# Kernel optimization log

Hardware: AMD Instinct MI355X
Metric: run time of the kernel (lower is better)

## Reference

```python
import jax, jax.numpy as jnp
import numpy as np

B, S, D = 2, 2048, 2048
H, KVH, DH = 16, 4, 128  # n_heads, n_kv_heads, head_dim
N_REP = H // KVH
THETA = 10000.0


def setup_inputs() -> dict:
    key = jax.random.key(0)
    ks = jax.random.split(key, 6)
    x = jax.random.normal(ks[0], (B, S, D), dtype=jnp.float32)
    wq = jax.random.normal(ks[1], (H * DH, D), dtype=jnp.float32) * (D ** -0.5)
    wk = jax.random.normal(ks[2], (KVH * DH, D), dtype=jnp.float32) * (D ** -0.5)
    wv = jax.random.normal(ks[3], (KVH * DH, D), dtype=jnp.float32) * (D ** -0.5)
    wo = jax.random.normal(ks[4], (D, H * DH), dtype=jnp.float32) * (D ** -0.5)
    # RoPE frequencies (complex freqs -> cos/sin), shape [S, DH//2]
    inv_freq = 1.0 / (THETA ** (np.arange(0, DH, 2, dtype=np.float32) / DH))
    angles = np.arange(S, dtype=np.float32)[:, None] * inv_freq[None, :]
    freqs_cos = jnp.asarray(np.cos(angles))
    freqs_sin = jnp.asarray(np.sin(angles))
    # causal additive mask [1,1,S,S]
    neg = jnp.full((S, S), -1e9, dtype=jnp.float32)
    mask = jnp.triu(neg, k=1)[None, None]
    return {"x": x, "freqs_cos": freqs_cos, "freqs_sin": freqs_sin,
            "mask": mask, "wq": wq, "wk": wk, "wv": wv, "wo": wo}


def _rope(t, cos, sin):
    # t: [B,S,h,DH]; cos/sin: [S,DH//2] -> broadcast [1,S,1,DH//2]
    tp = t.reshape(*t.shape[:-1], -1, 2)
    tr, ti = tp[..., 0], tp[..., 1]
    c = cos[None, :, None, :]
    s = sin[None, :, None, :]
    out_r = tr * c - ti * s
    out_i = tr * s + ti * c
    return jnp.stack([out_r, out_i], axis=-1).reshape(t.shape)


def reference(x, freqs_cos, freqs_sin, mask, wq, wk, wv, wo):
    b, s, _ = x.shape
    xq = jnp.einsum('bsd,ed->bse', x, wq).reshape(b, s, H, DH)
    xk = jnp.einsum('bsd,ed->bse', x, wk).reshape(b, s, KVH, DH)
    xv = jnp.einsum('bsd,ed->bse', x, wv).reshape(b, s, KVH, DH)
    xq = _rope(xq, freqs_cos, freqs_sin)
    xk = _rope(xk, freqs_cos, freqs_sin)
    # GQA: repeat kv heads
    xk = jnp.repeat(xk, N_REP, axis=2)
    xv = jnp.repeat(xv, N_REP, axis=2)
    q = xq.transpose(0, 2, 1, 3)  # [B,H,S,DH]
    k = xk.transpose(0, 2, 1, 3)
    v = xv.transpose(0, 2, 1, 3)
    scores = jnp.einsum('bhqd,bhkd->bhqk', q, k) / jnp.sqrt(jnp.float32(DH))
    scores = scores + mask
    attn = jax.nn.softmax(scores.astype(jnp.float32), axis=-1).astype(q.dtype)
    out = jnp.einsum('bhqk,bhkd->bhqd', attn, v)
    out = out.transpose(0, 2, 1, 3).reshape(b, s, H * DH)
    return jnp.einsum('bse,de->bsd', out, wo)
```

## Files before the change

kernel.cpp:

```cpp
#include <hip/hip_runtime.h>

#define Bq   2
#define Sq   2048
#define Dq   2048
#define Hq   16
#define KVHq 4
#define DHq  128

typedef unsigned short u16;
typedef short  bf16x8 __attribute__((ext_vector_type(8)));
typedef float  f32x4  __attribute__((ext_vector_type(4)));
typedef float  f32x16 __attribute__((ext_vector_type(16)));
typedef unsigned short u16x2 __attribute__((ext_vector_type(2)));
typedef unsigned short u16x4 __attribute__((ext_vector_type(4)));

__device__ __forceinline__ u16 f2bf(float f) {
    unsigned u = __float_as_uint(f);
    u += 0x7fffu + ((u >> 16) & 1u);
    return (u16)(u >> 16);
}
__device__ __forceinline__ float bf2f(u16 s) {
    return __uint_as_float(((unsigned)s) << 16);
}

__global__ void cast_bf16(const float* __restrict__ in, u16* __restrict__ out, int n4) {
    int i = blockIdx.x * 256 + threadIdx.x;
    if (i >= n4) return;
    float4 v = ((const float4*)in)[i];
    u16x4 o;
    o.x = f2bf(v.x); o.y = f2bf(v.y); o.z = f2bf(v.z); o.w = f2bf(v.w);
    ((u16x4*)out)[i] = o;
}

__global__ void cast_weights(const float* __restrict__ wq, const float* __restrict__ wk,
                             const float* __restrict__ wv, const float* __restrict__ wo,
                             u16* __restrict__ wqb, u16* __restrict__ wkvb,
                             u16* __restrict__ wob) {
    int i = blockIdx.x * 256 + threadIdx.x;
    const float4* src; u16x4* dst; int off;
    if (i < 1048576)      { src = (const float4*)wq; dst = (u16x4*)wqb;  off = i; }
    else if (i < 1310720) { src = (const float4*)wk; dst = (u16x4*)wkvb; off = i - 1048576; }
    else if (i < 1572864) { src = (const float4*)wv; dst = (u16x4*)wkvb + 262144; off = i - 1310720; }
    else                  { src = (const float4*)wo; dst = (u16x4*)wob;  off = i - 1572864; }
    float4 v = src[off];
    u16x4 o;
    o.x = f2bf(v.x); o.y = f2bf(v.y); o.z = f2bf(v.z); o.w = f2bf(v.w);
    dst[off] = o;
}

__device__ __forceinline__ void async16(const void* g, void* l) {
    __builtin_amdgcn_global_load_lds(
        (const __attribute__((address_space(1))) unsigned*)g,
        (__attribute__((address_space(3))) unsigned*)l, 16, 0, 0);
}

__device__ __forceinline__ void stc(u16* p, float v)   { *p = f2bf(v); }
__device__ __forceinline__ void stc(float* p, float v) { *p = v; }

template <typename OutT>
__global__ __launch_bounds__(256) void gemm_nt(
    const u16* __restrict__ A, const u16* __restrict__ W, OutT* __restrict__ C,
    int M, int N, int K)
{
    __shared__ __align__(16) u16 lA[128 * 32];
    __shared__ __align__(16) u16 lB[128 * 32];

    const int t    = threadIdx.x;
    const int w    = t >> 6;
    const int lane = t & 63;
    const int lr   = lane & 15;
    const int quad = lane >> 4;
    const int wm   = (w >> 1) * 64, wn = (w & 1) * 64;
    const int bm   = blockIdx.x * 128, bn = blockIdx.y * 128;

    const u16* Ab = A + (size_t)bm * K;
    const u16* Wb = W + (size_t)bn * K;

    const int r0  = t >> 2;
    const int r1  = (256 + t) >> 2;
    const int kc0 = (t & 3) * 8;

    char* la0 = (char*)lA + w * 1024;
    char* la1 = (char*)lA + 4096 + w * 1024;
    char* lb0 = (char*)lB + w * 1024;
    char* lb1 = (char*)lB + 4096 + w * 1024;

    f32x4 acc[4][4] = {};

    for (int kt = 0; kt < K; kt += 32) {
        async16(Ab + (size_t)r0 * K + kt + kc0, la0);
        async16(Ab + (size_t)r1 * K + kt + kc0, la1);
        async16(Wb + (size_t)r0 * K + kt + kc0, lb0);
        async16(Wb + (size_t)r1 * K + kt + kc0, lb1);
        __syncthreads();

        bf16x8 af[4], bfr[4];
#pragma unroll
        for (int i = 0; i < 4; i++)
            af[i] = *(const bf16x8*)&lA[(wm + i * 16 + lr) * 32 + quad * 8];
#pragma unroll
        for (int j = 0; j < 4; j++)
            bfr[j] = *(const bf16x8*)&lB[(wn + j * 16 + lr) * 32 + quad * 8];
#pragma unroll
        for (int i = 0; i < 4; i++)
#pragma unroll
            for (int j = 0; j < 4; j++)
                acc[i][j] = __builtin_amdgcn_mfma_f32_16x16x32_bf16(af[i], bfr[j], acc[i][j], 0, 0, 0);
        __syncthreads();
    }

#pragma unroll
    for (int i = 0; i < 4; i++)
#pragma unroll
        for (int j = 0; j < 4; j++)
#pragma unroll
            for (int r = 0; r < 4; r++) {
                int gm = bm + wm + i * 16 + quad * 4 + r;
                int gn = bn + wn + j * 16 + lr;
                stc(C + (size_t)gm * N + gn, acc[i][j][r]);
            }
}

__global__ void rope_k(u16* __restrict__ T, const float* __restrict__ Cs,
                       const float* __restrict__ Sn, int lognh, int total) {
    int i = blockIdx.x * 256 + threadIdx.x;
    if (i >= total) return;
    int p  = i & 63;
    int sh = i >> 6;
    int s  = (sh >> lognh) & (Sq - 1);
    float c = Cs[s * 64 + p], sn = Sn[s * 64 + p];
    u16x2* ptr = ((u16x2*)T) + i;
    u16x2 v = *ptr;
    float tr = bf2f(v.x), ti = bf2f(v.y);
    u16x2 ov;
    ov.x = f2bf(tr * c - ti * sn);
    ov.y = f2bf(tr * sn + ti * c);
    *ptr = ov;
}

__global__ void rope_kv(u16* __restrict__ KV, const float* __restrict__ Cs,
                        const float* __restrict__ Sn, int total) {
    int i = blockIdx.x * 256 + threadIdx.x;
    if (i >= total) return;
    int p     = i & 63;
    int kvh   = (i >> 6) & 3;
    int token = i >> 8;
    int s     = token & (Sq - 1);
    float c = Cs[s * 64 + p], sn = Sn[s * 64 + p];
    u16x2* ptr = ((u16x2*)KV) + (size_t)token * 512 + kvh * 64 + p;
    u16x2 v = *ptr;
    float tr = bf2f(v.x), ti = bf2f(v.y);
    u16x2 ov;
    ov.x = f2bf(tr * c - ti * sn);
    ov.y = f2bf(tr * sn + ti * c);
    *ptr = ov;
}

__global__ void transpose_v_k(const u16* __restrict__ KV, u16* __restrict__ Vt) {
    __shared__ u16 tile[32][33];
    const int bk = blockIdx.z;
    const int b = bk >> 2, kvh = bk & 3;
    const int s0 = blockIdx.x * 32, d0 = blockIdx.y * 32;
    const int tx = threadIdx.x, ty = threadIdx.y;
    tile[ty][tx] = KV[(size_t)(b * Sq + s0 + ty) * 1024 + 512 + kvh * 128 + d0 + tx];
    __syncthreads();
    Vt[((size_t)bk * DHq + d0 + ty) * Sq + s0 + tx] = tile[tx][ty];
}

#define PSCALE 0.12753102f
#define PBIAS  17.31234049f

__global__ __launch_bounds__(256, 2) void flash_attn_sk2(
    const u16* __restrict__ Q, const u16* __restrict__ KV,
    const u16* __restrict__ Vt, float* __restrict__ Oc, float* __restrict__ Lc)
{
    __shared__ __align__(16) u16 kl[4 * 64 * 32];
    __shared__ __align__(16) u16 vl[2 * 128 * 32];
    __shared__ __align__(16) u16 pl[4][32 * 64];

    const int bh = blockIdx.x;
    const int b = bh >> 4, h = bh & 15;
    const int kvh = h >> 2;
    const int c = 39 - (int)blockIdx.y;
    int qt, ci, nc;
    if (c < 4)       { qt = c;                    ci = 0;            nc = 1; }
    else if (c < 12) { qt = 4  + ((c - 4) >> 1);  ci = (c - 4) & 1;  nc = 2; }
    else if (c < 24) { qt = 8  + (c - 12) / 3;    ci = (c - 12) % 3; nc = 3; }
    else             { qt = 12 + ((c - 24) >> 2); ci = (c - 24) & 3; nc = 4; }
    const int T  = 2 * (qt + 1);
    const int t0 = (ci * T) / nc, t1 = ((ci + 1) * T) / nc;

    const int tid = threadIdx.x;
    const int w = tid >> 6, lane = tid & 63;
    const int col = lane & 31, hi = lane >> 5;
    const int q0 = qt * 128 + w * 32;

    const u16* Qp = Q + (size_t)(b * Sq + q0 + col) * (Hq * DHq) + h * DHq + hi * 8;
    bf16x8 qf[8];
#pragma unroll
    for (int ks = 0; ks < 8; ks++) qf[ks] = *(const bf16x8*)(Qp + ks * 16);

    const u16* Kg = KV + (size_t)b * Sq * 1024 + kvh * DHq;
    const u16* Vg = Vt + (size_t)(b * KVHq + kvh) * DHq * Sq;

    const int srow = lane >> 2;
    const int swl  = ((lane & 3) ^ ((lane >> 3) & 3)) * 8;
    const int xsw  = (col >> 1) & 3;
    const int px   = col & 7;

    f32x16 o[4] = {};
    float lsum[16] = {};

    for (int kt = t0; kt < t1; kt++) {
        const int kb = kt * 64;
#pragma unroll
        for (int c4 = 0; c4 < 4; c4++) {
            const u16* g = Kg + (size_t)(kb + w * 16 + srow) * 1024 + c4 * 32 + swl;
            async16(g, (char*)kl + (c4 * 2048 + w * 512) * 2 + lane * 16);
        }
#pragma unroll
        for (int c4 = 0; c4 < 4; c4++) {
            const int g2 = c4 & 1, dbase = (c4 >> 1) * 64;
            const u16* g = Vg + (size_t)(dbase + w * 16 + srow) * Sq + kb + g2 * 32 + swl;
            async16(g, (char*)vl + (g2 * 4096 + (dbase + w * 16) * 32) * 2 + lane * 16);
        }
        __syncthreads();

        f32x16 s0 = {}, s1 = {};
#pragma unroll
        for (int ks = 0; ks < 8; ks++) {
            const int ch    = (((ks & 1) * 2 + hi) ^ xsw) * 8;
            const int kkbase = (ks >> 1) * 2048 + ch;
            bf16x8 k0 = *(const bf16x8*)&kl[kkbase + col * 32];
            bf16x8 k1 = *(const bf16x8*)&kl[kkbase + (32 + col) * 32];
            s0 = __builtin_amdgcn_mfma_f32_32x32x16_bf16(qf[ks], k0, s0, 0, 0, 0);
            s1 = __builtin_amdgcn_mfma_f32_32x32x16_bf16(qf[ks], k1, s1, 0, 0, 0);
        }

#pragma unroll
        for (int r = 0; r < 16; r++) {
            const int rloc = (r & 3) + 8 * (r >> 2) + 4 * hi;
            const int qg = q0 + rloc;
            float v0 = s0[r] * PSCALE - PBIAS;
            float v1 = s1[r] * PSCALE - PBIAS;
            float p0 = (kb + col      <= qg) ? exp2f(v0) : 0.f;
            float p1 = (kb + 32 + col <= qg) ? exp2f(v1) : 0.f;
            lsum[r] += p0 + p1;
            const int rx = rloc & 7;
            pl[w][rloc * 64 + (((col >> 3) ^ rx) * 8) + (col & 7)]       = f2bf(p0);
            pl[w][rloc * 64 + ((((col >> 3) + 4) ^ rx) * 8) + (col & 7)] = f2bf(p1);
        }

#pragma unroll
        for (int ks = 0; ks < 4; ks++) {
            bf16x8 pa = *(const bf16x8*)&pl[w][col * 64 + ((ks * 2 + hi) ^ px) * 8];
            const int vch   = (((ks & 1) * 2 + hi) ^ xsw) * 8;
            const int vbase = (ks >> 1) * 4096 + vch;
#pragma unroll
            for (int n = 0; n < 4; n++) {
                bf16x8 vf = *(const bf16x8*)&vl[vbase + (n * 32 + col) * 32];
                o[n] = __builtin_amdgcn_mfma_f32_32x32x16_bf16(pa, vf, o[n], 0, 0, 0);
            }
        }
        __syncthreads();
    }

    float* Ocb = Oc + (size_t)(bh * 40 + c) * 16384 + (size_t)w * 32 * 128;
    float* Lcb = Lc + (size_t)(bh * 40 + c) * 128 + w * 32;
#pragma unroll
    for (int r = 0; r < 16; r++) {
        const int rloc = (r & 3) + 8 * (r >> 2) + 4 * hi;
        float t = lsum[r];
        t += __shfl_xor(t, 1);
        t += __shfl_xor(t, 2);
        t += __shfl_xor(t, 4);
        t += __shfl_xor(t, 8);
        t += __shfl_xor(t, 16);
        if (col == 0) Lcb[rloc] = t;
#pragma unroll
        for (int n = 0; n < 4; n++)
            Ocb[rloc * 128 + n * 32 + col] = o[n][r];
    }
}

__global__ __launch_bounds__(256) void flash_reduce2(
    const float* __restrict__ Oc, const float* __restrict__ Lc, u16* __restrict__ AO)
{
    const int bh = blockIdx.x;
    const int qt = blockIdx.y;
    const int e  = blockIdx.z * 256 + threadIdx.x;
    const int row = e >> 5, col4 = e & 31;
    int cst, nc;
    if (qt < 4)       { cst = qt;                 nc = 1; }
    else if (qt < 8)  { cst = 4  + 2 * (qt - 4);  nc = 2; }
    else if (qt < 12) { cst = 12 + 3 * (qt - 8);  nc = 3; }
    else              { cst = 24 + 4 * (qt - 12); nc = 4; }
    f32x4 acc = {0.f, 0.f, 0.f, 0.f};
    float l = 0.f;
    for (int i = 0; i < nc; i++) {
        const size_t base = (size_t)(bh * 40 + cst + i);
        acc += ((const f32x4*)(Oc + base * 16384))[e];
        l   += Lc[base * 128 + row];
    }
    const float inv = 1.0f / l;
    const int b = bh >> 4, h = bh & 15;
    u16x4 ov;
    ov.x = f2bf(acc[0] * inv); ov.y = f2bf(acc[1] * inv);
    ov.z = f2bf(acc[2] * inv); ov.w = f2bf(acc[3] * inv);
    u16* dst = AO + (size_t)(b * Sq + qt * 128 + row) * (Hq * DHq) + h * DHq + col4 * 4;
    *(u16x4*)dst = ov;
}

__global__ __launch_bounds__(256) void flash_attn(
    const u16* __restrict__ Q, const u16* __restrict__ KV,
    const u16* __restrict__ Vt, u16* __restrict__ O)
{
    __shared__ __align__(16) u16 plds[4][16 * 72];
    const int bh = blockIdx.x;
    const int b = bh >> 4, h = bh & 15;
    const int kvh = h >> 2;
    const int w = threadIdx.x >> 6, lane = threadIdx.x & 63;
    const int lr = lane & 15, quad = lane >> 4;
    const int yy = gridDim.y - 1 - blockIdx.y;
    const int q0 = yy * 64 + w * 16;

    const u16* Qp = Q + (size_t)(b * Sq + q0 + lr) * (Hq * DHq) + h * DHq + quad * 8;
    bf16x8 qf[4];
#pragma unroll
    for (int kk = 0; kk < 4; kk++) qf[kk] = *(const bf16x8*)(Qp + kk * 32);

    const u16* Kp = KV + (size_t)b * Sq * 1024 + kvh * DHq;
    const u16* Vp = Vt + (size_t)(b * KVHq + kvh) * DHq * Sq;

    f32x4 o[8] = {};
    float lsum[4] = {0.f, 0.f, 0.f, 0.f};

    const int nt = (q0 + 16 + 63) >> 6;
    for (int kt = 0; kt < nt; kt++) {
        const int kb = kt * 64;
        f32x4 s[4] = {};
#pragma unroll
        for (int kk = 0; kk < 4; kk++) {
#pragma unroll
            for (int j = 0; j < 4; j++) {
                bf16x8 kf = *(const bf16x8*)(Kp + (size_t)(kb + j * 16 + lr) * 1024 + kk * 32 + quad * 8);
                s[j] = __builtin_amdgcn_mfma_f32_16x16x32_bf16(qf[kk], kf, s[j], 0, 0, 0);
            }
        }
#pragma unroll
        for (int r = 0; r < 4; r++) {
            const int qg = q0 + quad * 4 + r;
#pragma unroll
            for (int j = 0; j < 4; j++) {
                float v = s[j][r] * PSCALE - PBIAS;
                float p = (kb + j * 16 + lr <= qg) ? exp2f(v) : 0.f;
                lsum[r] += p;
                plds[w][(quad * 4 + r) * 72 + j * 16 + lr] = f2bf(p);
            }
        }
        bf16x8 pa0 = *(const bf16x8*)&plds[w][lr * 72 + quad * 8];
        bf16x8 pa1 = *(const bf16x8*)&plds[w][lr * 72 + 32 + quad * 8];
#pragma unroll
        for (int dt = 0; dt < 8; dt++) {
            bf16x8 v0 = *(const bf16x8*)(Vp + (size_t)(dt * 16 + lr) * Sq + kb + quad * 8);
            bf16x8 v1 = *(const bf16x8*)(Vp + (size_t)(dt * 16 + lr) * Sq + kb + 32 + quad * 8);
            o[dt] = __builtin_amdgcn_mfma_f32_16x16x32_bf16(pa0, v0, o[dt], 0, 0, 0);
            o[dt] = __builtin_amdgcn_mfma_f32_16x16x32_bf16(pa1, v1, o[dt], 0, 0, 0);
        }
    }

    u16* Ob = O + (size_t)(b * Sq) * (Hq * DHq) + h * DHq;
#pragma unroll
    for (int r = 0; r < 4; r++) {
        float t = lsum[r];
        t += __shfl_xor(t, 1);
        t += __shfl_xor(t, 2);
        t += __shfl_xor(t, 4);
        t += __shfl_xor(t, 8);
        const float inv = 1.0f / t;
        const int qg = q0 + quad * 4 + r;
#pragma unroll
        for (int dt = 0; dt < 8; dt++)
            Ob[(size_t)qg * (Hq * DHq) + dt * 16 + lr] = f2bf(o[dt][r] * inv);
    }
}

extern "C" void kernel_launch(void* const* d_in, const int* in_sizes, int n_in,
                              void* d_out, int out_size, void* d_ws, size_t ws_size,
                              hipStream_t stream) {
    const float* x  = (const float*)d_in[0];
    const float* fc = (const float*)d_in[1];
    const float* fs = (const float*)d_in[2];
    const float* wq = (const float*)d_in[4];
    const float* wk = (const float*)d_in[5];
    const float* wv = (const float*)d_in[6];
    const float* wo = (const float*)d_in[7];
    float* out = (float*)d_out;

    char* ws = (char*)d_ws;
    u16* xb   = (u16*)(ws);
    u16* wqb  = (u16*)(ws + 16777216);
    u16* wkvb = (u16*)(ws + 25165824);
    u16* wob  = (u16*)(ws + 29360128);
    u16* Qb   = (u16*)(ws + 37748736);
    u16* KVb  = (u16*)(ws + 54525952);
    u16* Vtb  = (u16*)(ws + 62914560);
    u16* AOb  = (u16*)(ws + 67108864);
    float* Ocb = (float*)(ws + 83886080);
    float* Lcb = (float*)(ws + 167772160);
    const size_t WS_NEED = 168427520;

    cast_bf16<<<8192, 256, 0, stream>>>(x, xb, 2097152);
    cast_weights<<<10240, 256, 0, stream>>>(wq, wk, wv, wo, wqb, wkvb, wob);

    dim3 blk(256);
    gemm_nt<u16><<<dim3(32, 16), blk, 0, stream>>>(xb, wqb,  Qb,  4096, 2048, 2048);
    gemm_nt<u16><<<dim3(32, 8),  blk, 0, stream>>>(xb, wkvb, KVb, 4096, 1024, 2048);

    rope_k<<<16384, 256, 0, stream>>>(Qb, fc, fs, 4, 4194304);
    rope_kv<<<4096, 256, 0, stream>>>(KVb, fc, fs, 1048576);

    transpose_v_k<<<dim3(64, 4, 8), dim3(32, 32), 0, stream>>>(KVb, Vtb);

    if (ws_size >= WS_NEED) {
        flash_attn_sk2<<<dim3(32, 40), blk, 0, stream>>>(Qb, KVb, Vtb, Ocb, Lcb);
        flash_reduce2<<<dim3(32, 16, 16), blk, 0, stream>>>(Ocb, Lcb, AOb);
    } else {
        flash_attn<<<dim3(32, 32), blk, 0, stream>>>(Qb, KVb, Vtb, AOb);
    }

    gemm_nt<float><<<dim3(32, 16), blk, 0, stream>>>(AOb, wob, out, 4096, 2048, 2048);
}
```

Baseline: 392.1 us.

## Double-buffer K/V tiles and keep softmax P in registers via transposed QK

```diff
diff --git a/kernel.cpp b/kernel.cpp
--- a/kernel.cpp
+++ b/kernel.cpp
@@ -13,6 +13,7 @@
 typedef float  f32x16 __attribute__((ext_vector_type(16)));
 typedef unsigned short u16x2 __attribute__((ext_vector_type(2)));
 typedef unsigned short u16x4 __attribute__((ext_vector_type(4)));
+typedef unsigned uu32x4 __attribute__((ext_vector_type(4)));
 
 __device__ __forceinline__ u16 f2bf(float f) {
     unsigned u = __float_as_uint(f);
@@ -21,6 +22,19 @@
 }
 __device__ __forceinline__ float bf2f(u16 s) {
     return __uint_as_float(((unsigned)s) << 16);
+}
+
+__device__ __forceinline__ unsigned cvtpk(float a, float b) {
+    unsigned r;
+    asm("v_cvt_pk_bf16_f32 %0, %1, %2" : "=v"(r) : "v"(a), "v"(b));
+    return r;
+}
+__device__ __forceinline__ void pl32swap(unsigned& a, unsigned& b) {
+    asm("v_permlane32_swap_b32 %0, %1" : "+v"(a), "+v"(b));
+}
+__device__ __forceinline__ bf16x8 mkfrag(unsigned w0, unsigned w1, unsigned w2, unsigned w3) {
+    uu32x4 t = {w0, w1, w2, w3};
+    return __builtin_bit_cast(bf16x8, t);
 }
 
 __global__ void cast_bf16(const float* __restrict__ in, u16* __restrict__ out, int n4) {
@@ -174,9 +188,8 @@
     const u16* __restrict__ Q, const u16* __restrict__ KV,
     const u16* __restrict__ Vt, float* __restrict__ Oc, float* __restrict__ Lc)
 {
-    __shared__ __align__(16) u16 kl[4 * 64 * 32];
-    __shared__ __align__(16) u16 vl[2 * 128 * 32];
-    __shared__ __align__(16) u16 pl[4][32 * 64];
+    __shared__ __align__(16) u16 kl[2][4 * 64 * 32];
+    __shared__ __align__(16) u16 vl[2][2 * 128 * 32];
 
     const int bh = blockIdx.x;
     const int b = bh >> 4, h = bh & 15;
@@ -194,8 +207,9 @@
     const int w = tid >> 6, lane = tid & 63;
     const int col = lane & 31, hi = lane >> 5;
     const int q0 = qt * 128 + w * 32;
-
-    const u16* Qp = Q + (size_t)(b * Sq + q0 + col) * (Hq * DHq) + h * DHq + hi * 8;
+    const int qg = q0 + col;
+
+    const u16* Qp = Q + (size_t)(b * Sq + qg) * (Hq * DHq) + h * DHq + hi * 8;
     bf16x8 qf[8];
 #pragma unroll
     for (int ks = 0; ks < 8; ks++) qf[ks] = *(const bf16x8*)(Qp + ks * 16);
@@ -206,77 +220,110 @@
     const int srow = lane >> 2;
     const int swl  = ((lane & 3) ^ ((lane >> 3) & 3)) * 8;
     const int xsw  = (col >> 1) & 3;
-    const int px   = col & 7;
 
     f32x16 o[4] = {};
-    float lsum[16] = {};
-
-    for (int kt = t0; kt < t1; kt++) {
+    float lsum = 0.f;
+
+    auto STAGE = [&](int kt, int bsel) {
         const int kb = kt * 64;
 #pragma unroll
         for (int c4 = 0; c4 < 4; c4++) {
             const u16* g = Kg + (size_t)(kb + w * 16 + srow) * 1024 + c4 * 32 + swl;
-            async16(g, (char*)kl + (c4 * 2048 + w * 512) * 2 + lane * 16);
+            async16(g, (char*)kl[bsel] + (c4 * 2048 + w * 512) * 2 + lane * 16);
         }
 #pragma unroll
         for (int c4 = 0; c4 < 4; c4++) {
             const int g2 = c4 & 1, dbase = (c4 >> 1) * 64;
             const u16* g = Vg + (size_t)(dbase + w * 16 + srow) * Sq + kb + g2 * 32 + swl;
-            async16(g, (char*)vl + (g2 * 4096 + (dbase + w * 16) * 32) * 2 + lane * 16);
-        }
-        __syncthreads();
+            async16(g, (char*)vl[bsel] + (g2 * 4096 + (dbase + w * 16) * 32) * 2 + lane * 16);
+        }
+    };
+
+    STAGE(t0, 0);
+    __syncthreads();
+
+    int cur = 0;
+    for (int kt = t0; kt < t1; kt++) {
+        if (kt + 1 < t1) STAGE(kt + 1, cur ^ 1);
+
+        const int kb = kt * 64;
+        const u16* klc = kl[cur];
+        const u16* vlc = vl[cur];
 
         f32x16 s0 = {}, s1 = {};
+        __builtin_amdgcn_s_setprio(1);
 #pragma unroll
         for (int ks = 0; ks < 8; ks++) {
-            const int ch    = (((ks & 1) * 2 + hi) ^ xsw) * 8;
+            const int ch     = (((ks & 1) * 2 + hi) ^ xsw) * 8;
             const int kkbase = (ks >> 1) * 2048 + ch;
-            bf16x8 k0 = *(const bf16x8*)&kl[kkbase + col * 32];
-            bf16x8 k1 = *(const bf16x8*)&kl[kkbase + (32 + col) * 32];
-            s0 = __builtin_amdgcn_mfma_f32_32x32x16_bf16(qf[ks], k0, s0, 0, 0, 0);
-            s1 = __builtin_amdgcn_mfma_f32_32x32x16_bf16(qf[ks], k1, s1, 0, 0, 0);
-        }
-
-#pragma unroll
-        for (int r = 0; r < 16; r++) {
-            const int rloc = (r & 3) + 8 * (r >> 2) + 4 * hi;
-            const int qg = q0 + rloc;
-            float v0 = s0[r] * PSCALE - PBIAS;
-            float v1 = s1[r] * PSCALE - PBIAS;
-            float p0 = (kb + col      <= qg) ? exp2f(v0) : 0.f;
-            float p1 = (kb + 32 + col <= qg) ? exp2f(v1) : 0.f;
-            lsum[r] += p0 + p1;
-            const int rx = rloc & 7;
-            pl[w][rloc * 64 + (((col >> 3) ^ rx) * 8) + (col & 7)]       = f2bf(p0);
-            pl[w][rloc * 64 + ((((col >> 3) + 4) ^ rx) * 8) + (col & 7)] = f2bf(p1);
-        }
-
-#pragma unroll
-        for (int ks = 0; ks < 4; ks++) {
-            bf16x8 pa = *(const bf16x8*)&pl[w][col * 64 + ((ks * 2 + hi) ^ px) * 8];
-            const int vch   = (((ks & 1) * 2 + hi) ^ xsw) * 8;
-            const int vbase = (ks >> 1) * 4096 + vch;
-#pragma unroll
-            for (int n = 0; n < 4; n++) {
-                bf16x8 vf = *(const bf16x8*)&vl[vbase + (n * 32 + col) * 32];
-                o[n] = __builtin_amdgcn_mfma_f32_32x32x16_bf16(pa, vf, o[n], 0, 0, 0);
+            bf16x8 k0 = *(const bf16x8*)&klc[kkbase + col * 32];
+            bf16x8 k1 = *(const bf16x8*)&klc[kkbase + (32 + col) * 32];
+            s0 = __builtin_amdgcn_mfma_f32_32x32x16_bf16(k0, qf[ks], s0, 0, 0, 0);
+            s1 = __builtin_amdgcn_mfma_f32_32x32x16_bf16(k1, qf[ks], s1, 0, 0, 0);
+        }
+        __builtin_amdgcn_s_setprio(0);
+
+        float p0a[16], p1a[16];
+        float ls = 0.f;
+        if (q0 - kb >= 63) {
+#pragma unroll
+            for (int r = 0; r < 16; r++) {
+                float a0 = exp2f(s0[r] * PSCALE - PBIAS);
+                float a1 = exp2f(s1[r] * PSCALE - PBIAS);
+                ls += a0 + a1;
+                p0a[r] = a0; p1a[r] = a1;
             }
-        }
-        __syncthreads();
-    }
-
+        } else {
+            const int thr = qg - kb;
+#pragma unroll
+            for (int r = 0; r < 16; r++) {
+                const int kloc = (r & 3) + 8 * (r >> 2) + 4 * hi;
+                float a0 = (kloc <= thr)      ? exp2f(s0[r] * PSCALE - PBIAS) : 0.f;
+                float a1 = (kloc + 32 <= thr) ? exp2f(s1[r] * PSCALE - PBIAS) : 0.f;
+                ls += a0 + a1;
+                p0a[r] = a0; p1a[r] = a1;
+            }
+        }
+        lsum += ls;
+
+        __builtin_amdgcn_s_setprio(1);
+#define PV_HALF(PARR, KSBASE)                                                      \
+        {                                                                          \
+            _Pragma("unroll")                                                      \
+            for (int k2 = 0; k2 < 2; k2++) {                                       \
+                const int bb = k2 * 8;                                             \
+                unsigned wa = cvtpk(PARR[bb + 0], PARR[bb + 1]);                   \
+                unsigned wb = cvtpk(PARR[bb + 4], PARR[bb + 5]);                   \
+                pl32swap(wa, wb);                                                  \
+                unsigned wc = cvtpk(PARR[bb + 2], PARR[bb + 3]);                   \
+                unsigned wd = cvtpk(PARR[bb + 6], PARR[bb + 7]);                   \
+                pl32swap(wc, wd);                                                  \
+                bf16x8 pa = mkfrag(wa, wc, wb, wd);                                \
+                const int vch   = ((k2 * 2 + hi) ^ xsw) * 8;                       \
+                const int vbase = (((KSBASE) >> 1) * 4096) + vch;                  \
+                _Pragma("unroll")                                                  \
+                for (int n = 0; n < 4; n++) {                                      \
+                    bf16x8 vf = *(const bf16x8*)&vlc[vbase + (n * 32 + col) * 32]; \
+                    o[n] = __builtin_amdgcn_mfma_f32_32x32x16_bf16(pa, vf, o[n], 0, 0, 0); \
+                }                                                                  \
+            }                                                                      \
+        }
+        PV_HALF(p0a, 0)
+        PV_HALF(p1a, 2)
+#undef PV_HALF
+        __builtin_amdgcn_s_setprio(0);
+
+        if (kt + 1 < t1) __syncthreads();
+        cur ^= 1;
+    }
+
+    float tot = lsum + __shfl_xor(lsum, 32);
     float* Ocb = Oc + (size_t)(bh * 40 + c) * 16384 + (size_t)w * 32 * 128;
     float* Lcb = Lc + (size_t)(bh * 40 + c) * 128 + w * 32;
+    if (hi == 0) Lcb[col] = tot;
 #pragma unroll
     for (int r = 0; r < 16; r++) {
         const int rloc = (r & 3) + 8 * (r >> 2) + 4 * hi;
-        float t = lsum[r];
-        t += __shfl_xor(t, 1);
-        t += __shfl_xor(t, 2);
-        t += __shfl_xor(t, 4);
-        t += __shfl_xor(t, 8);
-        t += __shfl_xor(t, 16);
-        if (col == 0) Lcb[rloc] = t;
 #pragma unroll
         for (int n = 0; n < 4; n++)
             Ocb[rloc * 128 + n * 32 + col] = o[n][r];
```

Result: faster. 381.4 us (-2.7%).
